# Optimization experiments

Hardware: AMD Instinct MI355X
Metric: run time of the kernel (lower is better)

Reference implementation:

```python
import jax, jax.numpy as jnp
import numpy as np

B, D, H = 8192, 1024, 1024

def setup_inputs() -> dict:
    key = jax.random.key(0)
    ks = jax.random.split(key, 7)
    s_x = 1.0 / np.sqrt(D)
    s_h = 1.0 / np.sqrt(H)
    return {
        "e_t": jax.random.normal(ks[0], (B, D), jnp.float32),
        "h_prev": jax.random.normal(ks[1], (B, H), jnp.float32),
        "c_prev": jax.random.normal(ks[2], (B, H), jnp.float32),
        # gates concatenated in order (f, i, o, c), each block of size H
        "W_x": jax.random.uniform(ks[3], (4 * H, D), jnp.float32, -s_x, s_x),
        "b_x": jax.random.uniform(ks[4], (4 * H,), jnp.float32, -s_x, s_x),
        "W_h": jax.random.uniform(ks[5], (4 * H, H), jnp.float32, -s_h, s_h),
        "b_h": jax.random.uniform(ks[6], (4 * H,), jnp.float32, -s_h, s_h),
        "b_extra": jnp.zeros((4 * H,), jnp.float32),  # the b_f/b_i/b_o/b_c Parameters
    }

def reference(e_t, h_prev, c_prev, W_x, b_x, W_h, b_h, b_extra):
    # two fused GEMMs: [B,D]@[D,4H] and [B,H]@[H,4H]
    z = (jnp.einsum('bd,gd->bg', e_t, W_x)
         + jnp.einsum('bh,gh->bg', h_prev, W_h)
         + b_x + b_h + b_extra)  # [B, 4H]
    zf, zi, zo, zc = jnp.split(z, 4, axis=-1)
    g_t = jax.nn.sigmoid(zf)   # forget gate
    p_t = jax.nn.sigmoid(zi)   # input gate
    q_t = jax.nn.sigmoid(zo)   # output gate
    m_t_hat = jnp.tanh(zc)     # candidate cell
    c_t = g_t * c_prev + p_t * m_t_hat
    h_t = q_t * jnp.tanh(c_t)
    return (h_t, c_t)
```

## Files before the change

### kernel.cpp

```cpp
#include <hip/hip_runtime.h>
#include <stdint.h>

#define B_ROWS 8192
#define DH     1024
#define KTOT   2048
#define NTOT   4096

typedef __attribute__((ext_vector_type(8))) __bf16 bf16x8;
typedef __attribute__((ext_vector_type(4))) float  f32x4;

__device__ __forceinline__ unsigned short f2bf(float f) {
    unsigned int u = __float_as_uint(f);
    u += 0x7FFFu + ((u >> 16) & 1u);
    return (unsigned short)(u >> 16);
}

__device__ __forceinline__ float fast_sigmoid(float x) {
    return 1.0f / (1.0f + __expf(-x));
}
__device__ __forceinline__ float fast_tanh(float x) {
    float e = __expf(fminf(-2.0f * x, 80.0f));
    return (1.0f - e) / (1.0f + e);
}
__device__ __forceinline__ float sel4(float g0, float g1, float g2, float g3, int u) {
    float r = g0;
    r = (u == 1) ? g1 : r;
    r = (u == 2) ? g2 : r;
    r = (u == 3) ? g3 : r;
    return r;
}

#define NBLK_A (B_ROWS)
#define NBLK_W (NTOT)
#define NBLK_BIAS (NTOT / 256)

__global__ __launch_bounds__(256) void pack_all(const float* __restrict__ e_t,
                                                const float* __restrict__ h_prev,
                                                const float* __restrict__ W_x,
                                                const float* __restrict__ W_h,
                                                const float* __restrict__ b_x,
                                                const float* __restrict__ b_h,
                                                const float* __restrict__ b_e,
                                                unsigned short* __restrict__ A_cat,
                                                unsigned short* __restrict__ W_cat,
                                                float* __restrict__ bias) {
    const int blk = blockIdx.x;
    const int t   = threadIdx.x;
    if (blk < NBLK_A + NBLK_W) {
        const float* src0;
        unsigned short* dst;
        int row;
        if (blk < NBLK_A) {
            row = blk;
            src0 = nullptr;
            dst = A_cat + (size_t)row * KTOT;
            int c8 = t << 3;
            src0 = (c8 < DH) ? (e_t + (size_t)row * DH + c8)
                             : (h_prev + (size_t)row * DH + (c8 - DH));
        } else {
            row = blk - NBLK_A;
            int h = row >> 2, gate = row & 3;
            int srow = gate * DH + h;
            dst = W_cat + (size_t)row * KTOT;
            int c8 = t << 3;
            src0 = (c8 < DH) ? (W_x + (size_t)srow * DH + c8)
                             : (W_h + (size_t)srow * DH + (c8 - DH));
        }
        float4 f0 = ((const float4*)src0)[0];
        float4 f1 = ((const float4*)src0)[1];
        uint4 o;
        o.x = (unsigned)f2bf(f0.x) | ((unsigned)f2bf(f0.y) << 16);
        o.y = (unsigned)f2bf(f0.z) | ((unsigned)f2bf(f0.w) << 16);
        o.z = (unsigned)f2bf(f1.x) | ((unsigned)f2bf(f1.y) << 16);
        o.w = (unsigned)f2bf(f1.z) | ((unsigned)f2bf(f1.w) << 16);
        *(uint4*)(dst + t * 8) = o;
    } else {
        int gp = (blk - NBLK_A - NBLK_W) * 256 + t;
        int h = gp >> 2, gate = gp & 3;
        int g = gate * DH + h;
        bias[gp] = b_x[g] + b_h[g] + b_e[g];
    }
}

__global__ __launch_bounds__(256) void lstm_gemm(const unsigned short* __restrict__ A,
                                                 const unsigned short* __restrict__ Wc,
                                                 const float* __restrict__ bias,
                                                 const float* __restrict__ c_prev,
                                                 float* __restrict__ h_out,
                                                 float* __restrict__ c_out) {
    __shared__ __align__(16) unsigned char As[128 * 64 * 2];
    __shared__ __align__(16) unsigned char Bs[128 * 64 * 2];

    const int tid = threadIdx.x;
    const int w   = tid >> 6;
    const int l   = tid & 63;
    const int wm  = w >> 1, wn = w & 1;
    const int m0  = blockIdx.y * 128;
    const int n0  = blockIdx.x * 128;

    f32x4 acc[4][4];
#pragma unroll
    for (int i = 0; i < 4; ++i)
#pragma unroll
        for (int j = 0; j < 4; ++j) acc[i][j] = {0.f, 0.f, 0.f, 0.f};

    const int srow = w * 32 + (l >> 3);
    const int scol = (((l & 7) ^ ((l >> 3) & 7))) * 8;
    const unsigned short* gA = A  + (size_t)(m0 + srow) * KTOT + scol;
    const unsigned short* gB = Wc + (size_t)(n0 + srow) * KTOT + scol;
    unsigned char* lA = As + w * 4096;
    unsigned char* lB = Bs + w * 4096;

    const int lane15 = l & 15;
    const int quad   = l >> 4;
    const int xg0 = ((0 * 4 + quad) ^ (lane15 & 7)) * 16;
    const int xg1 = ((1 * 4 + quad) ^ (lane15 & 7)) * 16;

    for (int kt = 0; kt < KTOT / 64; ++kt) {
#pragma unroll
        for (int i = 0; i < 4; ++i) {
            __builtin_amdgcn_global_load_lds(
                (const __attribute__((address_space(1))) void*)(gA + (size_t)(i * 8) * KTOT + kt * 64),
                (__attribute__((address_space(3))) void*)(lA + i * 1024), 16, 0, 0);
            __builtin_amdgcn_global_load_lds(
                (const __attribute__((address_space(1))) void*)(gB + (size_t)(i * 8) * KTOT + kt * 64),
                (__attribute__((address_space(3))) void*)(lB + i * 1024), 16, 0, 0);
        }
        __syncthreads();

#pragma unroll
        for (int ks = 0; ks < 2; ++ks) {
            const int xg = ks ? xg1 : xg0;
            bf16x8 af[4], bfr[4];
#pragma unroll
            for (int mi = 0; mi < 4; ++mi)
                af[mi] = *(const bf16x8*)(As + (wm * 64 + mi * 16 + lane15) * 128 + xg);
#pragma unroll
            for (int ni = 0; ni < 4; ++ni)
                bfr[ni] = *(const bf16x8*)(Bs + (wn * 64 + ni * 16 + lane15) * 128 + xg);
#pragma unroll
            for (int mi = 0; mi < 4; ++mi)
#pragma unroll
                for (int ni = 0; ni < 4; ++ni)
                    acc[mi][ni] = __builtin_amdgcn_mfma_f32_16x16x32_bf16(af[mi], bfr[ni], acc[mi][ni], 0, 0, 0);
        }
        __syncthreads();
    }

    float biasv[4];
#pragma unroll
    for (int nj = 0; nj < 4; ++nj)
        biasv[nj] = bias[n0 + wn * 64 + nj * 16 + lane15];

    const int u = (l >> 2) & 3;
    const int v = l & 3;
    const int src_base = (l & 0x30) | (v << 2);
    const int hbase = (n0 + wn * 64) >> 2;

#pragma unroll
    for (int mi = 0; mi < 4; ++mi) {
        const int m = m0 + wm * 64 + mi * 16 + quad * 4 + u;
#pragma unroll
        for (int nj = 0; nj < 4; ++nj) {
            f32x4 a = acc[mi][nj];
            float bb = biasv[nj];
            float a0 = a[0] + bb, a1 = a[1] + bb, a2 = a[2] + bb, a3 = a[3] + bb;

            float s0, s1, s2, s3;
            s0 = __shfl(a0, src_base | 0, 64); s1 = __shfl(a1, src_base | 0, 64);
            s2 = __shfl(a2, src_base | 0, 64); s3 = __shfl(a3, src_base | 0, 64);
            float zf = sel4(s0, s1, s2, s3, u);
            s0 = __shfl(a0, src_base | 1, 64); s1 = __shfl(a1, src_base | 1, 64);
            s2 = __shfl(a2, src_base | 1, 64); s3 = __shfl(a3, src_base | 1, 64);
            float zi = sel4(s0, s1, s2, s3, u);
            s0 = __shfl(a0, src_base | 2, 64); s1 = __shfl(a1, src_base | 2, 64);
            s2 = __shfl(a2, src_base | 2, 64); s3 = __shfl(a3, src_base | 2, 64);
            float zo = sel4(s0, s1, s2, s3, u);
            s0 = __shfl(a0, src_base | 3, 64); s1 = __shfl(a1, src_base | 3, 64);
            s2 = __shfl(a2, src_base | 3, 64); s3 = __shfl(a3, src_base | 3, 64);
            float zc = sel4(s0, s1, s2, s3, u);

            float gf = fast_sigmoid(zf);
            float gi = fast_sigmoid(zi);
            float go = fast_sigmoid(zo);
            float mh = fast_tanh(zc);

            const int h = hbase + nj * 4 + v;
            const size_t off = (size_t)m * DH + h;
            float cp = c_prev[off];
            float ct = gf * cp + gi * mh;
            float ht = go * fast_tanh(ct);
            h_out[off] = ht;
            c_out[off] = ct;
        }
    }
}

extern "C" void kernel_launch(void* const* d_in, const int* in_sizes, int n_in,
                              void* d_out, int out_size, void* d_ws, size_t ws_size,
                              hipStream_t stream) {
    const float* e_t     = (const float*)d_in[0];
    const float* h_prev  = (const float*)d_in[1];
    const float* c_prev  = (const float*)d_in[2];
    const float* W_x     = (const float*)d_in[3];
    const float* b_x     = (const float*)d_in[4];
    const float* W_h     = (const float*)d_in[5];
    const float* b_h     = (const float*)d_in[6];
    const float* b_extra = (const float*)d_in[7];

    float* h_out = (float*)d_out;
    float* c_out = h_out + (size_t)B_ROWS * DH;

    unsigned short* A_cat = (unsigned short*)d_ws;
    unsigned short* W_cat = (unsigned short*)((char*)d_ws + (size_t)B_ROWS * KTOT * 2);
    float*          bias  = (float*)((char*)d_ws + (size_t)B_ROWS * KTOT * 2 + (size_t)NTOT * KTOT * 2);

    pack_all<<<NBLK_A + NBLK_W + NBLK_BIAS, 256, 0, stream>>>(
        e_t, h_prev, W_x, W_h, b_x, b_h, b_extra, A_cat, W_cat, bias);
    lstm_gemm<<<dim3(NTOT / 128, B_ROWS / 128), 256, 0, stream>>>(
        A_cat, W_cat, bias, c_prev, h_out, c_out);
}
```

Measured before the change: 350.7 us.

## Rewrite GEMM mainloop as 256x256 double-buffered pipelined tile with 8 waves

The GEMM kernel moves from a 128x128 tile with 4 waves and single-buffered LDS to a 256x256 tile with 8 waves, two LDS buffers, and async global-to-LDS prefetch of tile kt+2 interleaved with the MFMA phases. Explicit barriers, scheduling barriers, vmcnt waits and s_setprio are meant to hide load latency behind MFMA work and to raise operand reuse per byte loaded. The trade-offs are 128KB of LDS per block, a heavier accumulator register load, and fewer blocks overall, which may limit occupancy and tail balance.

```diff
diff --git a/kernel.cpp b/kernel.cpp
--- a/kernel.cpp
+++ b/kernel.cpp
@@ -52,7 +52,6 @@
         int row;
         if (blk < NBLK_A) {
             row = blk;
-            src0 = nullptr;
             dst = A_cat + (size_t)row * KTOT;
             int c8 = t << 3;
             src0 = (c8 < DH) ? (e_t + (size_t)row * DH + c8)
@@ -82,70 +81,183 @@
     }
 }
 
-__global__ __launch_bounds__(256) void lstm_gemm(const unsigned short* __restrict__ A,
-                                                 const unsigned short* __restrict__ Wc,
-                                                 const float* __restrict__ bias,
-                                                 const float* __restrict__ c_prev,
-                                                 float* __restrict__ h_out,
-                                                 float* __restrict__ c_out) {
-    __shared__ __align__(16) unsigned char As[128 * 64 * 2];
-    __shared__ __align__(16) unsigned char Bs[128 * 64 * 2];
+
+#define GLL(srcp, dstp) \
+    __builtin_amdgcn_global_load_lds( \
+        (const __attribute__((address_space(1))) void*)(srcp), \
+        (__attribute__((address_space(3))) void*)(dstp), 16, 0, 0)
+
+#define STAGE_HALF(g, buf, h, kt) do { \
+    GLL((g) + ((size_t)((h) * 128)      * KTOT) + (size_t)(kt) * 64, (buf) + (((h) * 128)      + w8) * 128); \
+    GLL((g) + ((size_t)((h) * 128 + 64) * KTOT) + (size_t)(kt) * 64, (buf) + (((h) * 128 + 64) + w8) * 128); \
+} while (0)
+
+#define PHASE_MID() do { \
+    __builtin_amdgcn_sched_barrier(0); \
+    __builtin_amdgcn_s_barrier(); \
+    asm volatile("s_waitcnt lgkmcnt(0)" ::: "memory"); \
+    __builtin_amdgcn_sched_barrier(0); \
+} while (0)
+
+#define PHASE_END() do { \
+    __builtin_amdgcn_sched_barrier(0); \
+    __builtin_amdgcn_s_barrier(); \
+    __builtin_amdgcn_sched_barrier(0); \
+} while (0)
+
+template <int MODE>
+__device__ __forceinline__ void do_tile(
+    int kt,
+    unsigned char* As_cur, unsigned char* Bs_cur,
+    const unsigned short* __restrict__ gA, const unsigned short* __restrict__ gB,
+    int w8, int rowA, int rowB, int xg0, int xg1,
+    f32x4 (&acc)[8][4])
+{
+    bf16x8 afl[4][2], afh[4][2], bfl[2][2], bfh[2][2];
+
+#pragma unroll
+    for (int mi = 0; mi < 4; ++mi) {
+        afl[mi][0] = *(const bf16x8*)(As_cur + rowA + mi * 2048 + xg0);
+        afl[mi][1] = *(const bf16x8*)(As_cur + rowA + mi * 2048 + xg1);
+    }
+#pragma unroll
+    for (int ni = 0; ni < 2; ++ni) {
+        bfl[ni][0] = *(const bf16x8*)(Bs_cur + rowB + ni * 2048 + xg0);
+        bfl[ni][1] = *(const bf16x8*)(Bs_cur + rowB + ni * 2048 + xg1);
+    }
+    PHASE_MID();
+    __builtin_amdgcn_s_setprio(1);
+#pragma unroll
+    for (int mi = 0; mi < 4; ++mi)
+#pragma unroll
+        for (int ni = 0; ni < 2; ++ni) {
+            acc[mi][ni] = __builtin_amdgcn_mfma_f32_16x16x32_bf16(afl[mi][0], bfl[ni][0], acc[mi][ni], 0, 0, 0);
+            acc[mi][ni] = __builtin_amdgcn_mfma_f32_16x16x32_bf16(afl[mi][1], bfl[ni][1], acc[mi][ni], 0, 0, 0);
+        }
+    __builtin_amdgcn_s_setprio(0);
+    PHASE_END();
+
+#pragma unroll
+    for (int ni = 0; ni < 2; ++ni) {
+        bfh[ni][0] = *(const bf16x8*)(Bs_cur + rowB + (2 + ni) * 2048 + xg0);
+        bfh[ni][1] = *(const bf16x8*)(Bs_cur + rowB + (2 + ni) * 2048 + xg1);
+    }
+    PHASE_MID();
+    __builtin_amdgcn_s_setprio(1);
+#pragma unroll
+    for (int mi = 0; mi < 4; ++mi)
+#pragma unroll
+        for (int ni = 0; ni < 2; ++ni) {
+            acc[mi][2 + ni] = __builtin_amdgcn_mfma_f32_16x16x32_bf16(afl[mi][0], bfh[ni][0], acc[mi][2 + ni], 0, 0, 0);
+            acc[mi][2 + ni] = __builtin_amdgcn_mfma_f32_16x16x32_bf16(afl[mi][1], bfh[ni][1], acc[mi][2 + ni], 0, 0, 0);
+        }
+    __builtin_amdgcn_s_setprio(0);
+    PHASE_END();
+
+#pragma unroll
+    for (int mi = 0; mi < 4; ++mi) {
+        afh[mi][0] = *(const bf16x8*)(As_cur + rowA + (4 + mi) * 2048 + xg0);
+        afh[mi][1] = *(const bf16x8*)(As_cur + rowA + (4 + mi) * 2048 + xg1);
+    }
+    if constexpr (MODE == 2) {
+        STAGE_HALF(gB, Bs_cur, 0, kt + 2);
+        STAGE_HALF(gB, Bs_cur, 1, kt + 2);
+    }
+    PHASE_MID();
+    __builtin_amdgcn_s_setprio(1);
+#pragma unroll
+    for (int mi = 0; mi < 4; ++mi)
+#pragma unroll
+        for (int ni = 0; ni < 2; ++ni) {
+            acc[4 + mi][ni] = __builtin_amdgcn_mfma_f32_16x16x32_bf16(afh[mi][0], bfl[ni][0], acc[4 + mi][ni], 0, 0, 0);
+            acc[4 + mi][ni] = __builtin_amdgcn_mfma_f32_16x16x32_bf16(afh[mi][1], bfl[ni][1], acc[4 + mi][ni], 0, 0, 0);
+        }
+    __builtin_amdgcn_s_setprio(0);
+    PHASE_END();
+
+    if constexpr (MODE == 2) {
+        STAGE_HALF(gA, As_cur, 0, kt + 2);
+        STAGE_HALF(gA, As_cur, 1, kt + 2);
+        __builtin_amdgcn_sched_barrier(0);
+        asm volatile("s_waitcnt vmcnt(8)" ::: "memory");
+        __builtin_amdgcn_sched_barrier(0);
+    } else if constexpr (MODE == 1) {
+        __builtin_amdgcn_sched_barrier(0);
+        asm volatile("s_waitcnt vmcnt(0)" ::: "memory");
+        __builtin_amdgcn_sched_barrier(0);
+    }
+    PHASE_MID();
+    __builtin_amdgcn_s_setprio(1);
+#pragma unroll
+    for (int mi = 0; mi < 4; ++mi)
+#pragma unroll
+        for (int ni = 0; ni < 2; ++ni) {
+            acc[4 + mi][2 + ni] = __builtin_amdgcn_mfma_f32_16x16x32_bf16(afh[mi][0], bfh[ni][0], acc[4 + mi][2 + ni], 0, 0, 0);
+            acc[4 + mi][2 + ni] = __builtin_amdgcn_mfma_f32_16x16x32_bf16(afh[mi][1], bfh[ni][1], acc[4 + mi][2 + ni], 0, 0, 0);
+        }
+    __builtin_amdgcn_s_setprio(0);
+    PHASE_END();
+}
+
+__global__ __launch_bounds__(512, 2) void lstm_gemm(
+    const unsigned short* __restrict__ A,
+    const unsigned short* __restrict__ Wc,
+    const float* __restrict__ bias,
+    const float* __restrict__ c_prev,
+    float* __restrict__ h_out,
+    float* __restrict__ c_out)
+{
+    __shared__ __align__(16) unsigned char lds[131072];
 
     const int tid = threadIdx.x;
     const int w   = tid >> 6;
     const int l   = tid & 63;
-    const int wm  = w >> 1, wn = w & 1;
-    const int m0  = blockIdx.y * 128;
-    const int n0  = blockIdx.x * 128;
-
-    f32x4 acc[4][4];
-#pragma unroll
-    for (int i = 0; i < 4; ++i)
+    const int wm  = w >> 2, wn = w & 3;
+    const int m0  = blockIdx.y * 256;
+    const int n0  = blockIdx.x * 256;
+    const int w8  = w * 8;
+
+    f32x4 acc[8][4];
+#pragma unroll
+    for (int i = 0; i < 8; ++i)
 #pragma unroll
         for (int j = 0; j < 4; ++j) acc[i][j] = {0.f, 0.f, 0.f, 0.f};
 
-    const int srow = w * 32 + (l >> 3);
-    const int scol = (((l & 7) ^ ((l >> 3) & 7))) * 8;
+    const int srow = w8 + (l >> 3);
+    const int scol = ((l & 7) ^ ((l >> 3) & 7)) * 8;
     const unsigned short* gA = A  + (size_t)(m0 + srow) * KTOT + scol;
     const unsigned short* gB = Wc + (size_t)(n0 + srow) * KTOT + scol;
-    unsigned char* lA = As + w * 4096;
-    unsigned char* lB = Bs + w * 4096;
+
+    unsigned char* As0 = lds;
+    unsigned char* As1 = lds + 32768;
+    unsigned char* Bs0 = lds + 65536;
+    unsigned char* Bs1 = lds + 98304;
 
     const int lane15 = l & 15;
     const int quad   = l >> 4;
-    const int xg0 = ((0 * 4 + quad) ^ (lane15 & 7)) * 16;
-    const int xg1 = ((1 * 4 + quad) ^ (lane15 & 7)) * 16;
-
-    for (int kt = 0; kt < KTOT / 64; ++kt) {
-#pragma unroll
-        for (int i = 0; i < 4; ++i) {
-            __builtin_amdgcn_global_load_lds(
-                (const __attribute__((address_space(1))) void*)(gA + (size_t)(i * 8) * KTOT + kt * 64),
-                (__attribute__((address_space(3))) void*)(lA + i * 1024), 16, 0, 0);
-            __builtin_amdgcn_global_load_lds(
-                (const __attribute__((address_space(1))) void*)(gB + (size_t)(i * 8) * KTOT + kt * 64),
-                (__attribute__((address_space(3))) void*)(lB + i * 1024), 16, 0, 0);
-        }
-        __syncthreads();
-
-#pragma unroll
-        for (int ks = 0; ks < 2; ++ks) {
-            const int xg = ks ? xg1 : xg0;
-            bf16x8 af[4], bfr[4];
-#pragma unroll
-            for (int mi = 0; mi < 4; ++mi)
-                af[mi] = *(const bf16x8*)(As + (wm * 64 + mi * 16 + lane15) * 128 + xg);
-#pragma unroll
-            for (int ni = 0; ni < 4; ++ni)
-                bfr[ni] = *(const bf16x8*)(Bs + (wn * 64 + ni * 16 + lane15) * 128 + xg);
-#pragma unroll
-            for (int mi = 0; mi < 4; ++mi)
-#pragma unroll
-                for (int ni = 0; ni < 4; ++ni)
-                    acc[mi][ni] = __builtin_amdgcn_mfma_f32_16x16x32_bf16(af[mi], bfr[ni], acc[mi][ni], 0, 0, 0);
-        }
-        __syncthreads();
-    }
+    const int rowA = (wm * 128 + lane15) * 128;
+    const int rowB = (wn * 64  + lane15) * 128;
+    const int xg0  = ((0 + quad) ^ (lane15 & 7)) * 16;
+    const int xg1  = ((4 + quad) ^ (lane15 & 7)) * 16;
+
+    STAGE_HALF(gA, As0, 0, 0);
+    STAGE_HALF(gA, As0, 1, 0);
+    STAGE_HALF(gB, Bs0, 0, 0);
+    STAGE_HALF(gB, Bs0, 1, 0);
+    STAGE_HALF(gA, As1, 0, 1);
+    STAGE_HALF(gA, As1, 1, 1);
+    STAGE_HALF(gB, Bs1, 0, 1);
+    STAGE_HALF(gB, Bs1, 1, 1);
+    asm volatile("s_waitcnt vmcnt(8)" ::: "memory");
+    __builtin_amdgcn_s_barrier();
+
+#pragma unroll 1
+    for (int kt2 = 0; kt2 < 15; ++kt2) {
+        do_tile<2>(2 * kt2,     As0, Bs0, gA, gB, w8, rowA, rowB, xg0, xg1, acc);
+        do_tile<2>(2 * kt2 + 1, As1, Bs1, gA, gB, w8, rowA, rowB, xg0, xg1, acc);
+    }
+    do_tile<1>(30, As0, Bs0, gA, gB, w8, rowA, rowB, xg0, xg1, acc);
+    do_tile<0>(31, As1, Bs1, gA, gB, w8, rowA, rowB, xg0, xg1, acc);
 
     float biasv[4];
 #pragma unroll
@@ -158,8 +270,8 @@
     const int hbase = (n0 + wn * 64) >> 2;
 
 #pragma unroll
-    for (int mi = 0; mi < 4; ++mi) {
-        const int m = m0 + wm * 64 + mi * 16 + quad * 4 + u;
+    for (int mi = 0; mi < 8; ++mi) {
+        const int m = m0 + wm * 128 + mi * 16 + quad * 4 + u;
 #pragma unroll
         for (int nj = 0; nj < 4; ++nj) {
             f32x4 a = acc[mi][nj];
@@ -217,6 +329,6 @@
 
     pack_all<<<NBLK_A + NBLK_W + NBLK_BIAS, 256, 0, stream>>>(
         e_t, h_prev, W_x, W_h, b_x, b_h, b_extra, A_cat, W_cat, bias);
-    lstm_gemm<<<dim3(NTOT / 128, B_ROWS / 128), 256, 0, stream>>>(
+    lstm_gemm<<<dim3(NTOT / 256, B_ROWS / 256), 512, 0, stream>>>(
         A_cat, W_cat, bias, c_prev, h_out, c_out);
 }
```

Result: faster. 322.2 us (-8.1%).
